# Kernel optimization log

Hardware: AMD Instinct MI355X
Metric: run time of the kernel (lower is better)

The kernel has to match this reference:

```python
import jax, jax.numpy as jnp
import numpy as np


def setup_inputs() -> dict:
    key = jax.random.key(0)
    k1, k2 = jax.random.split(key)
    inputs = jax.random.normal(k1, (32768, 512), dtype=jnp.float32)
    codebook = jax.random.normal(k2, (8192, 512), dtype=jnp.float32)
    return {"inputs": inputs, "codebook": codebook}


def reference(inputs, codebook):
    # inputs: [N, D] (flattened), codebook: [K, D]
    D = codebook.shape[1]
    x = inputs.reshape(-1, D)                          # [N, D]
    cb_sqr = jnp.sum(codebook ** 2, axis=1)            # [K]
    x_sqr = jnp.sum(x ** 2, axis=1, keepdims=True)     # [N, 1]
    distances = (cb_sqr[None, :] + x_sqr) - 2.0 * jnp.einsum('nd,kd->nk', x, codebook)
    soft_distances = jax.nn.softmax(-distances, axis=1)  # [N, K]
    return soft_distances
```

## Files before the change

kernel.cpp:

```cpp
#include <hip/hip_runtime.h>


typedef __attribute__((ext_vector_type(8))) __bf16 bf16x8;
typedef __attribute__((ext_vector_type(4))) float f32x4;

typedef __attribute__((address_space(1))) const void global_cvoid;
typedef __attribute__((address_space(3))) void lds_void;

__device__ inline unsigned short f32_to_bf16_rne(float f) {
    unsigned int u = __float_as_uint(f);
    unsigned int r = u + 0x7FFFu + ((u >> 16) & 1u);
    return (unsigned short)(r >> 16);
}
__device__ inline float bf16u_to_f32(unsigned short h) {
    return __uint_as_float(((unsigned int)h) << 16);
}

__global__ void split_kernel(const float* __restrict__ in,
                             unsigned short* __restrict__ hi,
                             unsigned short* __restrict__ lo, int n4) {
    int i = blockIdx.x * blockDim.x + threadIdx.x;
    int stride = gridDim.x * blockDim.x;
    for (; i < n4; i += stride) {
        float4 v = reinterpret_cast<const float4*>(in)[i];
        float vv[4] = {v.x, v.y, v.z, v.w};
        ushort4 hv, lv;
        unsigned short h[4], l[4];
#pragma unroll
        for (int j = 0; j < 4; ++j) {
            h[j] = f32_to_bf16_rne(vv[j]);
            float r = vv[j] - bf16u_to_f32(h[j]);
            l[j] = f32_to_bf16_rne(r);
        }
        hv.x = h[0]; hv.y = h[1]; hv.z = h[2]; hv.w = h[3];
        lv.x = l[0]; lv.y = l[1]; lv.z = l[2]; lv.w = l[3];
        reinterpret_cast<ushort4*>(hi)[i] = hv;
        reinterpret_cast<ushort4*>(lo)[i] = lv;
    }
}

__global__ void rowsq_kernel(const float* __restrict__ cb, float* __restrict__ out) {
    int row = blockIdx.x * 4 + (threadIdx.x >> 6);
    int lane = threadIdx.x & 63;
    const float4* p = reinterpret_cast<const float4*>(cb + (size_t)row * 512);
    float4 a = p[lane];
    float4 b = p[lane + 64];
    float s = a.x * a.x + a.y * a.y + a.z * a.z + a.w * a.w +
              b.x * b.x + b.y * b.y + b.z * b.z + b.w * b.w;
#pragma unroll
    for (int o = 32; o >= 1; o >>= 1) s += __shfl_xor(s, o);
    if (lane == 0) out[row] = s;
}


#define RD_A(mq_, bq_)                                                            \
    { _Pragma("unroll") for (int m = 0; m < 4; ++m)                               \
        afr[m] = *(const bf16x8*)&lds[bq_][0][(a_slot + ((mq_)*4 + m) * 64) * 8]; }

#define RD_B(bq_)                                                                 \
    { _Pragma("unroll") for (int n = 0; n < 4; ++n)                               \
        bfr[n] = *(const bf16x8*)&lds[bq_][1][(b_slot + n * 64) * 8]; }

#define ST(tt_)                                                                   \
    { int prod_ = (tt_) >> 4, ko_ = ((tt_) & 15) * 32, bq_ = (tt_) & 3;           \
      const unsigned short* Asrc_ = (prod_ < 2 ? Ah : Al) + arow0 + ko_;          \
      const unsigned short* Bsrc_ = (prod_ == 1 ? Bl : Bh) + brow0 + ko_;         \
      _Pragma("unroll") for (int j = 0; j < 2; ++j) {                             \
          __builtin_amdgcn_global_load_lds((global_cvoid*)(Asrc_ + goff[j]),      \
              (lds_void*)&lds[bq_][0][sl8[j]], 16, 0, 0);                         \
          __builtin_amdgcn_global_load_lds((global_cvoid*)(Bsrc_ + goff[j]),      \
              (lds_void*)&lds[bq_][1][sl8[j]], 16, 0, 0);                         \
      } }

#define MM(mq_)                                                                   \
    { _Pragma("unroll") for (int m = 0; m < 4; ++m)                               \
      _Pragma("unroll") for (int n = 0; n < 4; ++n)                               \
          acc[(mq_) * 4 + m][n] = __builtin_amdgcn_mfma_f32_16x16x32_bf16(        \
              afr[m], bfr[n], acc[(mq_) * 4 + m][n], 0, 0, 0); }

#define MIDSYNC()                                                                 \
    { __builtin_amdgcn_s_barrier();                                               \
      asm volatile("s_waitcnt lgkmcnt(0)" ::: "memory"); }

template <int F16>
__global__ __launch_bounds__(512, 2) void gemm_kernel(
    const unsigned short* __restrict__ Ah, const unsigned short* __restrict__ Al,
    const unsigned short* __restrict__ Bh, const unsigned short* __restrict__ Bl,
    const float* __restrict__ cbq, float* __restrict__ outf,
    unsigned short* __restrict__ p16, float* __restrict__ max_part,
    float* __restrict__ sum_part) {
    __shared__ __align__(16) unsigned short lds[4][2][8192];

    const int t = threadIdx.x;
    const int lane = t & 63;
    const int w = t >> 6;
    const int wm = w >> 2, wn = w & 3;
    const int fr = lane & 15, fg = lane >> 4;

    int bid = blockIdx.x;
    int swz = (bid & 7) * 512 + (bid >> 3);
    const int bm = swz >> 5, bn = swz & 31;
    const int row0 = bm * 256, col0 = bn * 256;
    const size_t arow0 = (size_t)row0 * 512;
    const size_t brow0 = (size_t)col0 * 512;

    const int xsl = fg ^ ((fr >> 1) & 3);
    const int a_slot = (wm * 128 + fr) * 4 + xsl;
    const int b_slot = (wn * 64 + fr) * 4 + xsl;

    int goff[2], sl8[2];
#pragma unroll
    for (int j = 0; j < 2; ++j) {
        int s = j * 512 + t;
        int r_ = s >> 2, cp_ = s & 3;
        int cl_ = cp_ ^ ((r_ >> 1) & 3);
        goff[j] = r_ * 512 + cl_ * 8;
        sl8[j] = s * 8;
    }

    f32x4 acc[8][4] = {};
    bf16x8 afr[4], bfr[4];

    ST(0);
    ST(1);
    ST(2);
    asm volatile("s_waitcnt vmcnt(8)\n\ts_barrier" ::: "memory");

    for (int tt = 0; tt < 48; ++tt) {
        const int bq = tt & 3;
        RD_B(bq);
        RD_A(0, bq);
        if (tt < 45) ST(tt + 3);
        MIDSYNC();
        __builtin_amdgcn_s_setprio(1); MM(0); __builtin_amdgcn_s_setprio(0);
        __builtin_amdgcn_s_barrier();
        RD_A(1, bq);
        MIDSYNC();
        __builtin_amdgcn_s_setprio(1); MM(1); __builtin_amdgcn_s_setprio(0);
        if (tt < 45) {
            asm volatile("s_waitcnt vmcnt(8)\n\ts_barrier" ::: "memory");
        } else if (tt == 45) {
            asm volatile("s_waitcnt vmcnt(4)\n\ts_barrier" ::: "memory");
        } else if (tt == 46) {
            asm volatile("s_waitcnt vmcnt(0)\n\ts_barrier" ::: "memory");
        } else {
            __builtin_amdgcn_s_barrier();
        }
    }

    float* redm = (float*)&lds[0][0][0];
    float* reds = redm + 1024;

    float cq[4];
#pragma unroll
    for (int n = 0; n < 4; ++n) cq[n] = cbq[col0 + wn * 64 + n * 16 + fr];
#pragma unroll
    for (int m = 0; m < 8; ++m)
#pragma unroll
        for (int n = 0; n < 4; ++n)
#pragma unroll
            for (int r = 0; r < 4; ++r)
                acc[m][n][r] = 2.0f * acc[m][n][r] - cq[n];

    float rmx[8][4];
#pragma unroll
    for (int m = 0; m < 8; ++m)
#pragma unroll
        for (int r = 0; r < 4; ++r) {
            float v = fmaxf(fmaxf(acc[m][0][r], acc[m][1][r]),
                            fmaxf(acc[m][2][r], acc[m][3][r]));
#pragma unroll
            for (int o = 1; o < 16; o <<= 1) v = fmaxf(v, __shfl_xor(v, o));
            rmx[m][r] = v;
        }
    __syncthreads();
    if (fr == 0) {
#pragma unroll
        for (int m = 0; m < 8; ++m)
#pragma unroll
            for (int r = 0; r < 4; ++r)
                redm[wn * 256 + wm * 128 + m * 16 + fg * 4 + r] = rmx[m][r];
    }
    __syncthreads();
#pragma unroll
    for (int m = 0; m < 8; ++m)
#pragma unroll
        for (int r = 0; r < 4; ++r) {
            int row = wm * 128 + m * 16 + fg * 4 + r;
            rmx[m][r] = fmaxf(fmaxf(redm[row], redm[256 + row]),
                              fmaxf(redm[512 + row], redm[768 + row]));
        }
#pragma unroll
    for (int m = 0; m < 8; ++m)
#pragma unroll
        for (int r = 0; r < 4; ++r) {
            float s = 0.f;
#pragma unroll
            for (int n = 0; n < 4; ++n) s += __expf(acc[m][n][r] - rmx[m][r]);
#pragma unroll
            for (int o = 1; o < 16; o <<= 1) s += __shfl_xor(s, o);
            if (fr == 0) reds[wn * 256 + wm * 128 + m * 16 + fg * 4 + r] = s;
        }
    __syncthreads();
    if (wn == 0 && fr == 0) {
#pragma unroll
        for (int m = 0; m < 8; ++m)
#pragma unroll
            for (int r = 0; r < 4; ++r) {
                int row = wm * 128 + m * 16 + fg * 4 + r;
                size_t gr = (size_t)(row0 + row);
                max_part[gr * 32 + bn] = rmx[m][r];
                sum_part[gr * 32 + bn] =
                    reds[row] + reds[256 + row] + reds[512 + row] + reds[768 + row];
            }
    }
#pragma unroll
    for (int m = 0; m < 8; ++m)
#pragma unroll
        for (int n = 0; n < 4; ++n)
#pragma unroll
            for (int r = 0; r < 4; ++r) {
                size_t gr = (size_t)(row0 + wm * 128 + m * 16 + fg * 4 + r);
                size_t gi = gr * 8192 + col0 + wn * 64 + n * 16 + fr;
                if constexpr (F16) {
                    union { _Float16 h; unsigned short u; } cv;
                    cv.h = (_Float16)__expf(acc[m][n][r] - rmx[m][r]);
                    p16[gi] = cv.u;
                } else {
                    outf[gi] = acc[m][n][r];
                }
            }
}

__global__ void combine_kernel(const float* __restrict__ max_part,
                               const float* __restrict__ sum_part,
                               float* __restrict__ row_m, float* __restrict__ row_is,
                               float* __restrict__ scale, int do_scale) {
    int row = blockIdx.x * 8 + (threadIdx.x >> 5);
    int l = threadIdx.x & 31;
    size_t off = (size_t)row * 32 + l;
    float m = max_part[off];
    float s = sum_part[off];
    float gm = m;
#pragma unroll
    for (int o = 16; o >= 1; o >>= 1) gm = fmaxf(gm, __shfl_xor(gm, o, 32));
    float c = s * __expf(m - gm);
#pragma unroll
    for (int o = 16; o >= 1; o >>= 1) c += __shfl_xor(c, o, 32);
    float inv = 1.0f / c;
    if (do_scale) scale[off] = __expf(m - gm) * inv;
    if (l == 0) {
        row_m[row] = gm;
        row_is[row] = inv;
    }
}

__global__ void norm_kernel(float* __restrict__ out, const float* __restrict__ row_m,
                            const float* __restrict__ row_is) {
    size_t i = (size_t)blockIdx.x * blockDim.x + threadIdx.x;
    size_t stride = (size_t)gridDim.x * blockDim.x;
    const size_t n4 = 268435456ull / 4;
    float4* p = reinterpret_cast<float4*>(out);
    for (; i < n4; i += stride) {
        int row = (int)(i >> 11);
        float m = row_m[row];
        float is = row_is[row];
        float4 v = p[i];
        v.x = __expf(v.x - m) * is;
        v.y = __expf(v.y - m) * is;
        v.z = __expf(v.z - m) * is;
        v.w = __expf(v.w - m) * is;
        p[i] = v;
    }
}

__global__ void norm_f16_kernel(const unsigned short* __restrict__ p16,
                                const float* __restrict__ scale,
                                float* __restrict__ out) {
    size_t i = (size_t)blockIdx.x * blockDim.x + threadIdx.x;
    size_t stride = (size_t)gridDim.x * blockDim.x;
    const size_t ng = 268435456ull / 8;
    const uint4* src = reinterpret_cast<const uint4*>(p16);
    float4* dst = reinterpret_cast<float4*>(out);
    for (; i < ng; i += stride) {
        int row = (int)(i >> 10);
        int bn = (int)((i >> 5) & 31);
        float s = scale[(size_t)row * 32 + bn];
        union { uint4 u; _Float16 h[8]; } cv;
        cv.u = src[i];
        float4 o1, o2;
        o1.x = (float)cv.h[0] * s; o1.y = (float)cv.h[1] * s;
        o1.z = (float)cv.h[2] * s; o1.w = (float)cv.h[3] * s;
        o2.x = (float)cv.h[4] * s; o2.y = (float)cv.h[5] * s;
        o2.z = (float)cv.h[6] * s; o2.w = (float)cv.h[7] * s;
        dst[i * 2] = o1;
        dst[i * 2 + 1] = o2;
    }
}

extern "C" void kernel_launch(void* const* d_in, const int* in_sizes, int n_in,
                              void* d_out, int out_size, void* d_ws, size_t ws_size,
                              hipStream_t stream) {
    const float* x = (const float*)d_in[0];
    const float* cb = (const float*)d_in[1];
    float* out = (float*)d_out;
    char* ws = (char*)d_ws;

    unsigned short* Xh = (unsigned short*)(ws);
    unsigned short* Xl = (unsigned short*)(ws + 33554432ull);
    unsigned short* Ch = (unsigned short*)(ws + 67108864ull);
    unsigned short* Cl = (unsigned short*)(ws + 75497472ull);
    float* cbq       = (float*)(ws + 83886080ull);
    float* max_part  = (float*)(ws + 83918848ull);
    float* sum_part  = (float*)(ws + 88113152ull);
    float* row_m     = (float*)(ws + 92307456ull);
    float* row_is    = (float*)(ws + 92438528ull);
    float* scale     = (float*)(ws + 92569600ull);
    unsigned short* p16 = (unsigned short*)(ws + 96763904ull);

    const bool f16path = (ws_size >= 633634816ull);

    split_kernel<<<2048, 256, 0, stream>>>(x, Xh, Xl, 32768 * 512 / 4);
    split_kernel<<<1024, 256, 0, stream>>>(cb, Ch, Cl, 8192 * 512 / 4);
    rowsq_kernel<<<2048, 256, 0, stream>>>(cb, cbq);
    if (f16path) {
        gemm_kernel<1><<<4096, 512, 0, stream>>>(Xh, Xl, Ch, Cl, cbq, out, p16,
                                                 max_part, sum_part);
        combine_kernel<<<4096, 256, 0, stream>>>(max_part, sum_part, row_m, row_is,
                                                 scale, 1);
        norm_f16_kernel<<<4096, 256, 0, stream>>>(p16, scale, out);
    } else {
        gemm_kernel<0><<<4096, 512, 0, stream>>>(Xh, Xl, Ch, Cl, cbq, out, p16,
                                                 max_part, sum_part);
        combine_kernel<<<4096, 256, 0, stream>>>(max_part, sum_part, row_m, row_is,
                                                 scale, 0);
        norm_kernel<<<4096, 256, 0, stream>>>(out, row_m, row_is);
    }
}
```

Baseline: 1.438 ms.

## Shrink GEMM tile to 128x256 with double buffering for higher occupancy

Halves the M tile of the split-bf16 distance GEMM from 256 to 128 rows, cuts the LDS ring from four stages to two, and raises launch bounds from 2 to 4 blocks per CU, with twice as many blocks launched. The pipeline becomes a simple one-ahead prefetch with a full vmcnt(0) wait and barrier each K step, replacing the split-M MFMA phases and their priority tweaks. The aim is more resident waves to hide latency, at the cost of less codebook reuse per block, more global traffic, and a shallower prefetch pipeline.

Result: slower. 1.468 ms (+2.0%).

```diff
diff --git a/kernel.cpp b/kernel.cpp
--- a/kernel.cpp
+++ b/kernel.cpp
@@ -53,43 +53,40 @@
 }
 
 
-#define RD_A(mq_, bq_)                                                            \
+#define RD_A(bq_)                                                                 \
     { _Pragma("unroll") for (int m = 0; m < 4; ++m)                               \
-        afr[m] = *(const bf16x8*)&lds[bq_][0][(a_slot + ((mq_)*4 + m) * 64) * 8]; }
+        afr[m] = *(const bf16x8*)&ldsA[bq_][(a_slot + m * 64) * 8]; }
 
 #define RD_B(bq_)                                                                 \
     { _Pragma("unroll") for (int n = 0; n < 4; ++n)                               \
-        bfr[n] = *(const bf16x8*)&lds[bq_][1][(b_slot + n * 64) * 8]; }
+        bfr[n] = *(const bf16x8*)&ldsB[bq_][(b_slot + n * 64) * 8]; }
 
 #define ST(tt_)                                                                   \
-    { int prod_ = (tt_) >> 4, ko_ = ((tt_) & 15) * 32, bq_ = (tt_) & 3;           \
+    { int prod_ = (tt_) >> 4, ko_ = ((tt_) & 15) * 32, bq_ = (tt_) & 1;           \
       const unsigned short* Asrc_ = (prod_ < 2 ? Ah : Al) + arow0 + ko_;          \
       const unsigned short* Bsrc_ = (prod_ == 1 ? Bl : Bh) + brow0 + ko_;         \
-      _Pragma("unroll") for (int j = 0; j < 2; ++j) {                             \
-          __builtin_amdgcn_global_load_lds((global_cvoid*)(Asrc_ + goff[j]),      \
-              (lds_void*)&lds[bq_][0][sl8[j]], 16, 0, 0);                         \
-          __builtin_amdgcn_global_load_lds((global_cvoid*)(Bsrc_ + goff[j]),      \
-              (lds_void*)&lds[bq_][1][sl8[j]], 16, 0, 0);                         \
-      } }
-
-#define MM(mq_)                                                                   \
+      __builtin_amdgcn_global_load_lds((global_cvoid*)(Asrc_ + goffA),            \
+          (lds_void*)&ldsA[bq_][slA], 16, 0, 0);                                  \
+      _Pragma("unroll") for (int j = 0; j < 2; ++j)                               \
+          __builtin_amdgcn_global_load_lds((global_cvoid*)(Bsrc_ + goffB[j]),     \
+              (lds_void*)&ldsB[bq_][slB[j]], 16, 0, 0);                           \
+    }
+
+#define MM_ALL()                                                                  \
     { _Pragma("unroll") for (int m = 0; m < 4; ++m)                               \
       _Pragma("unroll") for (int n = 0; n < 4; ++n)                               \
-          acc[(mq_) * 4 + m][n] = __builtin_amdgcn_mfma_f32_16x16x32_bf16(        \
-              afr[m], bfr[n], acc[(mq_) * 4 + m][n], 0, 0, 0); }
-
-#define MIDSYNC()                                                                 \
-    { __builtin_amdgcn_s_barrier();                                               \
-      asm volatile("s_waitcnt lgkmcnt(0)" ::: "memory"); }
+          acc[m][n] = __builtin_amdgcn_mfma_f32_16x16x32_bf16(                    \
+              afr[m], bfr[n], acc[m][n], 0, 0, 0); }
 
 template <int F16>
-__global__ __launch_bounds__(512, 2) void gemm_kernel(
+__global__ __launch_bounds__(512, 4) void gemm_kernel(
     const unsigned short* __restrict__ Ah, const unsigned short* __restrict__ Al,
     const unsigned short* __restrict__ Bh, const unsigned short* __restrict__ Bl,
     const float* __restrict__ cbq, float* __restrict__ outf,
     unsigned short* __restrict__ p16, float* __restrict__ max_part,
     float* __restrict__ sum_part) {
-    __shared__ __align__(16) unsigned short lds[4][2][8192];
+    __shared__ __align__(16) unsigned short ldsA[2][4096];
+    __shared__ __align__(16) unsigned short ldsB[2][8192];
 
     const int t = threadIdx.x;
     const int lane = t & 63;
@@ -98,73 +95,61 @@
     const int fr = lane & 15, fg = lane >> 4;
 
     int bid = blockIdx.x;
-    int swz = (bid & 7) * 512 + (bid >> 3);
+    int swz = (bid & 7) * 1024 + (bid >> 3);
     const int bm = swz >> 5, bn = swz & 31;
-    const int row0 = bm * 256, col0 = bn * 256;
+    const int row0 = bm * 128, col0 = bn * 256;
     const size_t arow0 = (size_t)row0 * 512;
     const size_t brow0 = (size_t)col0 * 512;
 
     const int xsl = fg ^ ((fr >> 1) & 3);
-    const int a_slot = (wm * 128 + fr) * 4 + xsl;
+    const int a_slot = (wm * 64 + fr) * 4 + xsl;
     const int b_slot = (wn * 64 + fr) * 4 + xsl;
 
-    int goff[2], sl8[2];
+    int goffA, slA, goffB[2], slB[2];
+    {
+        int s = t, r_ = s >> 2, cp_ = s & 3;
+        goffA = r_ * 512 + (cp_ ^ ((r_ >> 1) & 3)) * 8;
+        slA = s * 8;
+    }
 #pragma unroll
     for (int j = 0; j < 2; ++j) {
-        int s = j * 512 + t;
-        int r_ = s >> 2, cp_ = s & 3;
-        int cl_ = cp_ ^ ((r_ >> 1) & 3);
-        goff[j] = r_ * 512 + cl_ * 8;
-        sl8[j] = s * 8;
-    }
-
-    f32x4 acc[8][4] = {};
+        int s = j * 512 + t, r_ = s >> 2, cp_ = s & 3;
+        goffB[j] = r_ * 512 + (cp_ ^ ((r_ >> 1) & 3)) * 8;
+        slB[j] = s * 8;
+    }
+
+    f32x4 acc[4][4] = {};
     bf16x8 afr[4], bfr[4];
 
     ST(0);
-    ST(1);
-    ST(2);
-    asm volatile("s_waitcnt vmcnt(8)\n\ts_barrier" ::: "memory");
+    asm volatile("s_waitcnt vmcnt(0)\n\ts_barrier" ::: "memory");
 
     for (int tt = 0; tt < 48; ++tt) {
-        const int bq = tt & 3;
+        const int bq = tt & 1;
         RD_B(bq);
-        RD_A(0, bq);
-        if (tt < 45) ST(tt + 3);
-        MIDSYNC();
-        __builtin_amdgcn_s_setprio(1); MM(0); __builtin_amdgcn_s_setprio(0);
-        __builtin_amdgcn_s_barrier();
-        RD_A(1, bq);
-        MIDSYNC();
-        __builtin_amdgcn_s_setprio(1); MM(1); __builtin_amdgcn_s_setprio(0);
-        if (tt < 45) {
-            asm volatile("s_waitcnt vmcnt(8)\n\ts_barrier" ::: "memory");
-        } else if (tt == 45) {
-            asm volatile("s_waitcnt vmcnt(4)\n\ts_barrier" ::: "memory");
-        } else if (tt == 46) {
-            asm volatile("s_waitcnt vmcnt(0)\n\ts_barrier" ::: "memory");
-        } else {
-            __builtin_amdgcn_s_barrier();
-        }
-    }
-
-    float* redm = (float*)&lds[0][0][0];
-    float* reds = redm + 1024;
+        RD_A(bq);
+        if (tt < 47) ST(tt + 1);
+        MM_ALL();
+        asm volatile("s_waitcnt vmcnt(0)\n\ts_barrier" ::: "memory");
+    }
+
+    float* redm = (float*)&ldsA[0][0];
+    float* reds = redm + 512;
 
     float cq[4];
 #pragma unroll
     for (int n = 0; n < 4; ++n) cq[n] = cbq[col0 + wn * 64 + n * 16 + fr];
 #pragma unroll
-    for (int m = 0; m < 8; ++m)
+    for (int m = 0; m < 4; ++m)
 #pragma unroll
         for (int n = 0; n < 4; ++n)
 #pragma unroll
             for (int r = 0; r < 4; ++r)
                 acc[m][n][r] = 2.0f * acc[m][n][r] - cq[n];
 
-    float rmx[8][4];
-#pragma unroll
-    for (int m = 0; m < 8; ++m)
+    float rmx[4][4];
+#pragma unroll
+    for (int m = 0; m < 4; ++m)
 #pragma unroll
         for (int r = 0; r < 4; ++r) {
             float v = fmaxf(fmaxf(acc[m][0][r], acc[m][1][r]),
@@ -176,22 +161,22 @@
     __syncthreads();
     if (fr == 0) {
 #pragma unroll
-        for (int m = 0; m < 8; ++m)
+        for (int m = 0; m < 4; ++m)
 #pragma unroll
             for (int r = 0; r < 4; ++r)
-                redm[wn * 256 + wm * 128 + m * 16 + fg * 4 + r] = rmx[m][r];
+                redm[wn * 128 + wm * 64 + m * 16 + fg * 4 + r] = rmx[m][r];
     }
     __syncthreads();
 #pragma unroll
-    for (int m = 0; m < 8; ++m)
+    for (int m = 0; m < 4; ++m)
 #pragma unroll
         for (int r = 0; r < 4; ++r) {
-            int row = wm * 128 + m * 16 + fg * 4 + r;
-            rmx[m][r] = fmaxf(fmaxf(redm[row], redm[256 + row]),
-                              fmaxf(redm[512 + row], redm[768 + row]));
+            int row = wm * 64 + m * 16 + fg * 4 + r;
+            rmx[m][r] = fmaxf(fmaxf(redm[row], redm[128 + row]),
+                              fmaxf(redm[256 + row], redm[384 + row]));
         }
 #pragma unroll
-    for (int m = 0; m < 8; ++m)
+    for (int m = 0; m < 4; ++m)
 #pragma unroll
         for (int r = 0; r < 4; ++r) {
             float s = 0.f;
@@ -199,28 +184,28 @@
             for (int n = 0; n < 4; ++n) s += __expf(acc[m][n][r] - rmx[m][r]);
 #pragma unroll
             for (int o = 1; o < 16; o <<= 1) s += __shfl_xor(s, o);
-            if (fr == 0) reds[wn * 256 + wm * 128 + m * 16 + fg * 4 + r] = s;
+            if (fr == 0) reds[wn * 128 + wm * 64 + m * 16 + fg * 4 + r] = s;
         }
     __syncthreads();
     if (wn == 0 && fr == 0) {
 #pragma unroll
-        for (int m = 0; m < 8; ++m)
+        for (int m = 0; m < 4; ++m)
 #pragma unroll
             for (int r = 0; r < 4; ++r) {
-                int row = wm * 128 + m * 16 + fg * 4 + r;
+                int row = wm * 64 + m * 16 + fg * 4 + r;
                 size_t gr = (size_t)(row0 + row);
                 max_part[gr * 32 + bn] = rmx[m][r];
                 sum_part[gr * 32 + bn] =
-                    reds[row] + reds[256 + row] + reds[512 + row] + reds[768 + row];
+                    reds[row] + reds[128 + row] + reds[256 + row] + reds[384 + row];
             }
     }
 #pragma unroll
-    for (int m = 0; m < 8; ++m)
+    for (int m = 0; m < 4; ++m)
 #pragma unroll
         for (int n = 0; n < 4; ++n)
 #pragma unroll
             for (int r = 0; r < 4; ++r) {
-                size_t gr = (size_t)(row0 + wm * 128 + m * 16 + fg * 4 + r);
+                size_t gr = (size_t)(row0 + wm * 64 + m * 16 + fg * 4 + r);
                 size_t gi = gr * 8192 + col0 + wn * 64 + n * 16 + fr;
                 if constexpr (F16) {
                     union { _Float16 h; unsigned short u; } cv;
@@ -324,13 +309,13 @@
     split_kernel<<<1024, 256, 0, stream>>>(cb, Ch, Cl, 8192 * 512 / 4);
     rowsq_kernel<<<2048, 256, 0, stream>>>(cb, cbq);
     if (f16path) {
-        gemm_kernel<1><<<4096, 512, 0, stream>>>(Xh, Xl, Ch, Cl, cbq, out, p16,
+        gemm_kernel<1><<<8192, 512, 0, stream>>>(Xh, Xl, Ch, Cl, cbq, out, p16,
                                                  max_part, sum_part);
         combine_kernel<<<4096, 256, 0, stream>>>(max_part, sum_part, row_m, row_is,
                                                  scale, 1);
         norm_f16_kernel<<<4096, 256, 0, stream>>>(p16, scale, out);
     } else {
-        gemm_kernel<0><<<4096, 512, 0, stream>>>(Xh, Xl, Ch, Cl, cbq, out, p16,
+        gemm_kernel<0><<<8192, 512, 0, stream>>>(Xh, Xl, Ch, Cl, cbq, out, p16,
                                                  max_part, sum_part);
         combine_kernel<<<4096, 256, 0, stream>>>(max_part, sum_part, row_m, row_is,
                                                  scale, 0);
```

## Restructure GEMM main loop to triple-buffered single-phase MFMA with fewer barriers

Applied to the files above, without the earlier changes.

The LDS ring goes from four stages to three (96KB instead of 128KB), and the prefetch depth drops from three tiles ahead to two. Each iteration now reads all eight A fragments and four B fragments at once and issues all 32 MFMAs in one block. This removes the two mid-iteration barriers and the s_setprio ping-pong. The aim is to cut synchronization overhead and free LDS, at the cost of more VGPRs for fragments and less latency hiding with the shallower prefetch.

Result: no change. 1.410 ms (-1.9%).

```diff
diff --git a/kernel.cpp b/kernel.cpp
--- a/kernel.cpp
+++ b/kernel.cpp
@@ -53,34 +53,30 @@
 }
 
 
-#define RD_A(mq_, bq_)                                                            \
-    { _Pragma("unroll") for (int m = 0; m < 4; ++m)                               \
-        afr[m] = *(const bf16x8*)&lds[bq_][0][(a_slot + ((mq_)*4 + m) * 64) * 8]; }
+#define RD_A(bq_)                                                                 \
+    { _Pragma("unroll") for (int m = 0; m < 8; ++m)                               \
+        afr[m] = *(const bf16x8*)&ldsA[bq_][(a_slot + m * 64) * 8]; }
 
 #define RD_B(bq_)                                                                 \
     { _Pragma("unroll") for (int n = 0; n < 4; ++n)                               \
-        bfr[n] = *(const bf16x8*)&lds[bq_][1][(b_slot + n * 64) * 8]; }
-
-#define ST(tt_)                                                                   \
-    { int prod_ = (tt_) >> 4, ko_ = ((tt_) & 15) * 32, bq_ = (tt_) & 3;           \
+        bfr[n] = *(const bf16x8*)&ldsB[bq_][(b_slot + n * 64) * 8]; }
+
+#define ST(tt_, bq_)                                                              \
+    { int prod_ = (tt_) >> 4, ko_ = ((tt_) & 15) * 32;                            \
       const unsigned short* Asrc_ = (prod_ < 2 ? Ah : Al) + arow0 + ko_;          \
       const unsigned short* Bsrc_ = (prod_ == 1 ? Bl : Bh) + brow0 + ko_;         \
       _Pragma("unroll") for (int j = 0; j < 2; ++j) {                             \
           __builtin_amdgcn_global_load_lds((global_cvoid*)(Asrc_ + goff[j]),      \
-              (lds_void*)&lds[bq_][0][sl8[j]], 16, 0, 0);                         \
+              (lds_void*)&ldsA[bq_][sl8[j]], 16, 0, 0);                           \
           __builtin_amdgcn_global_load_lds((global_cvoid*)(Bsrc_ + goff[j]),      \
-              (lds_void*)&lds[bq_][1][sl8[j]], 16, 0, 0);                         \
+              (lds_void*)&ldsB[bq_][sl8[j]], 16, 0, 0);                           \
       } }
 
-#define MM(mq_)                                                                   \
-    { _Pragma("unroll") for (int m = 0; m < 4; ++m)                               \
+#define MM_ALL()                                                                  \
+    { _Pragma("unroll") for (int m = 0; m < 8; ++m)                               \
       _Pragma("unroll") for (int n = 0; n < 4; ++n)                               \
-          acc[(mq_) * 4 + m][n] = __builtin_amdgcn_mfma_f32_16x16x32_bf16(        \
-              afr[m], bfr[n], acc[(mq_) * 4 + m][n], 0, 0, 0); }
-
-#define MIDSYNC()                                                                 \
-    { __builtin_amdgcn_s_barrier();                                               \
-      asm volatile("s_waitcnt lgkmcnt(0)" ::: "memory"); }
+          acc[m][n] = __builtin_amdgcn_mfma_f32_16x16x32_bf16(                    \
+              afr[m], bfr[n], acc[m][n], 0, 0, 0); }
 
 template <int F16>
 __global__ __launch_bounds__(512, 2) void gemm_kernel(
@@ -89,7 +85,8 @@
     const float* __restrict__ cbq, float* __restrict__ outf,
     unsigned short* __restrict__ p16, float* __restrict__ max_part,
     float* __restrict__ sum_part) {
-    __shared__ __align__(16) unsigned short lds[4][2][8192];
+    __shared__ __align__(16) unsigned short ldsA[3][8192];
+    __shared__ __align__(16) unsigned short ldsB[3][8192];
 
     const int t = threadIdx.x;
     const int lane = t & 63;
@@ -111,44 +108,36 @@
     int goff[2], sl8[2];
 #pragma unroll
     for (int j = 0; j < 2; ++j) {
-        int s = j * 512 + t;
-        int r_ = s >> 2, cp_ = s & 3;
-        int cl_ = cp_ ^ ((r_ >> 1) & 3);
-        goff[j] = r_ * 512 + cl_ * 8;
+        int s = j * 512 + t, r_ = s >> 2, cp_ = s & 3;
+        goff[j] = r_ * 512 + (cp_ ^ ((r_ >> 1) & 3)) * 8;
         sl8[j] = s * 8;
     }
 
     f32x4 acc[8][4] = {};
-    bf16x8 afr[4], bfr[4];
-
-    ST(0);
-    ST(1);
-    ST(2);
-    asm volatile("s_waitcnt vmcnt(8)\n\ts_barrier" ::: "memory");
-
+    bf16x8 afr[8], bfr[4];
+
+    ST(0, 0);
+    ST(1, 1);
+    asm volatile("s_waitcnt vmcnt(4)\n\ts_barrier" ::: "memory");
+
+    int bq = 0, sq = 2;
     for (int tt = 0; tt < 48; ++tt) {
-        const int bq = tt & 3;
         RD_B(bq);
-        RD_A(0, bq);
-        if (tt < 45) ST(tt + 3);
-        MIDSYNC();
-        __builtin_amdgcn_s_setprio(1); MM(0); __builtin_amdgcn_s_setprio(0);
-        __builtin_amdgcn_s_barrier();
-        RD_A(1, bq);
-        MIDSYNC();
-        __builtin_amdgcn_s_setprio(1); MM(1); __builtin_amdgcn_s_setprio(0);
-        if (tt < 45) {
-            asm volatile("s_waitcnt vmcnt(8)\n\ts_barrier" ::: "memory");
-        } else if (tt == 45) {
-            asm volatile("s_waitcnt vmcnt(4)\n\ts_barrier" ::: "memory");
+        RD_A(bq);
+        if (tt < 46) ST(tt + 2, sq);
+        MM_ALL();
+        if (tt < 46) {
+            asm volatile("s_waitcnt vmcnt(4) lgkmcnt(0)\n\ts_barrier" ::: "memory");
         } else if (tt == 46) {
-            asm volatile("s_waitcnt vmcnt(0)\n\ts_barrier" ::: "memory");
+            asm volatile("s_waitcnt vmcnt(0) lgkmcnt(0)\n\ts_barrier" ::: "memory");
         } else {
-            __builtin_amdgcn_s_barrier();
-        }
-    }
-
-    float* redm = (float*)&lds[0][0][0];
+            asm volatile("s_waitcnt lgkmcnt(0)\n\ts_barrier" ::: "memory");
+        }
+        bq = (bq == 2) ? 0 : bq + 1;
+        sq = (sq == 2) ? 0 : sq + 1;
+    }
+
+    float* redm = (float*)&ldsA[0][0];
     float* reds = redm + 1024;
 
     float cq[4];
```
